# Kernel optimization log

Measured on AMD Instinct MI355X. Metric: run time of the kernel, lower is better.

The kernel has to match this reference:

```python
import jax, jax.numpy as jnp
import numpy as np

N = 100000       # nodes
E = 1600000      # edges (avg degree 16)
F_IN, H, C = 128, 128, 47


def setup_inputs() -> dict:
    key = jax.random.key(0)
    ks = jax.random.split(key, 12)
    def lin(k, fan_in, fan_out):
        return (jax.random.normal(k, (fan_in, fan_out), dtype=jnp.float32)
                / np.float32(np.sqrt(fan_in)))
    return {
        "x": jax.random.normal(ks[0], (N, F_IN), dtype=jnp.float32),
        "src": jax.random.randint(ks[1], (E,), 0, N, dtype=jnp.int32),
        "dst": jax.random.randint(ks[2], (E,), 0, N, dtype=jnp.int32),
        "w_self0": lin(ks[3], F_IN, H),
        "w_neigh0": lin(ks[4], F_IN, H),
        "b0": jnp.zeros((H,), jnp.float32),
        "w_self1": lin(ks[5], H, H),
        "w_neigh1": lin(ks[6], H, H),
        "b1": jnp.zeros((H,), jnp.float32),
        "w_self2": lin(ks[7], H, C),
        "w_neigh2": lin(ks[8], H, C),
        "b2": jnp.zeros((C,), jnp.float32),
    }


def _sage_layer(h, src, dst, w_self, w_neigh, b):
    # mean-aggregate neighbor features: gather h[src], scatter-add to dst
    agg = jax.ops.segment_sum(h[src], dst, num_segments=N)        # [N, d]
    deg = jax.ops.segment_sum(jnp.ones((src.shape[0], 1), h.dtype), dst,
                              num_segments=N)                     # [N, 1]
    mean = agg / jnp.maximum(deg, 1.0)
    # DGL SAGEConv('mean'): fc_self(h_dst) + fc_neigh(mean) + bias
    return h @ w_self + mean @ w_neigh + b


def reference(x, src, dst,
              w_self0, w_neigh0, b0,
              w_self1, w_neigh1, b1,
              w_self2, w_neigh2, b2):
    h = _sage_layer(x, src, dst, w_self0, w_neigh0, b0)
    h = jax.nn.relu(h)  # dropout is identity in eval mode
    h = _sage_layer(h, src, dst, w_self1, w_neigh1, b1)
    h = jax.nn.relu(h)
    h = _sage_layer(h, src, dst, w_self2, w_neigh2, b2)
    return h
```

## Files before the change

### kernel.cpp

```cpp
#include <hip/hip_runtime.h>

typedef unsigned int u32;
typedef unsigned short u16;
typedef __attribute__((ext_vector_type(8))) short short8;
typedef __attribute__((ext_vector_type(4))) float f32x4;

#define POOLCAP 65536
#define IDXMASK 0x1ffff

__device__ __forceinline__ u16 f2bf(float f) {
    u32 u = __float_as_uint(f);
    u32 r = (u + 0x7fffu + ((u >> 16) & 1u)) >> 16;
    return (u16)r;
}
__device__ __forceinline__ float bf2f(u32 lo16) { return __uint_as_float(lo16 << 16); }

__device__ __forceinline__ void acc_u4p(float2* a, uint4 v) {
    u32 w[4] = {v.x, v.y, v.z, v.w};
#pragma unroll
    for (int i = 0; i < 4; i++) {
        a[i].x += __uint_as_float(w[i] << 16);
        a[i].y += __uint_as_float(w[i] & 0xffff0000u);
    }
}


__global__ __launch_bounds__(256) void prep_w_all(const float* __restrict__ ws0, const float* __restrict__ wn0, u16* __restrict__ wt0,
                                                  const float* __restrict__ ws1, const float* __restrict__ wn1, u16* __restrict__ wt1,
                                                  const float* __restrict__ ws2, const float* __restrict__ wn2, u16* __restrict__ wt2) {
    int bid = blockIdx.x;
    const float *ws, *wn;
    u16* wt;
    int dout, HW, local;
    if (bid < 128)      { ws = ws0; wn = wn0; wt = wt0; dout = 128; HW = 128; local = bid; }
    else if (bid < 256) { ws = ws1; wn = wn1; wt = wt1; dout = 128; HW = 128; local = bid - 128; }
    else                { ws = ws2; wn = wn2; wt = wt2; dout = 47;  HW = 64;  local = bid - 256; }
    int idx = local * 256 + threadIdx.x;
    int n = idx >> 7, k = idx & 127;
    float v = 0.f;
    if (n < HW) { if (n < dout) v = ws[k * dout + n]; }
    else { int nn = n - HW; if (nn < dout) v = wn[k * dout + nn]; }
    wt[idx] = f2bf(v);
}


__global__ __launch_bounds__(256) void hist256(const int* __restrict__ dst,
                                               int* __restrict__ bcnt, int E) {
    __shared__ int bins[256];
    bins[threadIdx.x] = 0;
    __syncthreads();
    int gid = blockIdx.x * 256 + threadIdx.x;
    int stride = gridDim.x * 256;
    const int4* d4 = (const int4*)dst;
    int n4 = E >> 2;
    for (int k = gid; k < n4; k += stride) {
        int4 v = d4[k];
        atomicAdd(&bins[v.x >> 9], 1);
        atomicAdd(&bins[v.y >> 9], 1);
        atomicAdd(&bins[v.z >> 9], 1);
        atomicAdd(&bins[v.w >> 9], 1);
    }
    for (int k = (n4 << 2) + gid; k < E; k += stride)
        atomicAdd(&bins[dst[k] >> 9], 1);
    __syncthreads();
    int b = bins[threadIdx.x];
    if (b) atomicAdd(&bcnt[threadIdx.x], b);
}

__global__ __launch_bounds__(256) void scan256(const int* __restrict__ bcnt,
                                               int* __restrict__ boff,
                                               int* __restrict__ cursor) {
    __shared__ int sm[256];
    int t = threadIdx.x;
    int v = bcnt[t];
    sm[t] = v;
    __syncthreads();
    for (int off = 1; off < 256; off <<= 1) {
        int u = (t >= off) ? sm[t - off] : 0;
        __syncthreads();
        sm[t] += u;
        __syncthreads();
    }
    int excl = sm[t] - v;
    boff[t] = excl;
    cursor[t] = excl;
    if (t == 255) boff[256] = sm[255];
}

#define TILE 4096
__global__ __launch_bounds__(512) void bucket_scatter(const int* __restrict__ src,
                                                      const int* __restrict__ dst,
                                                      int* __restrict__ cursor,
                                                      uint2* __restrict__ pairs, int E) {
    __shared__ uint2 sp[TILE];
    __shared__ int s_cnt[256], s_off[256], s_gpos[256], s_cnt2[256];
    const int tid = threadIdx.x;
    const int base = blockIdx.x * TILE;
    const int tn = min(TILE, E - base);
    if (tid < 256) { s_cnt[tid] = 0; s_cnt2[tid] = 0; }
    __syncthreads();
    int d[8], s[8];
#pragma unroll
    for (int j = 0; j < 8; j++) {
        int k = tid + j * 512;
        if (k < tn) {
            d[j] = dst[base + k];
            s[j] = src[base + k];
            atomicAdd(&s_cnt[d[j] >> 9], 1);
        } else d[j] = -1;
    }
    __syncthreads();
    if (tid < 256) s_off[tid] = s_cnt[tid];
    __syncthreads();
    for (int off = 1; off < 256; off <<= 1) {
        int v = 0;
        if (tid < 256 && tid >= off) v = s_off[tid - off];
        __syncthreads();
        if (tid < 256) s_off[tid] += v;
        __syncthreads();
    }
    if (tid < 256 && s_cnt[tid] > 0) s_gpos[tid] = atomicAdd(&cursor[tid], s_cnt[tid]);
    __syncthreads();
#pragma unroll
    for (int j = 0; j < 8; j++) {
        if (d[j] >= 0) {
            int b = d[j] >> 9;
            int p = atomicAdd(&s_cnt2[b], 1);
            sp[s_off[b] - s_cnt[b] + p] = make_uint2((u32)d[j], (u32)s[j]);
        }
    }
    __syncthreads();
    for (int k = tid; k < tn; k += 512) {
        uint2 pr = sp[k];
        int b = (int)(pr.x >> 9);
        pairs[s_gpos[b] + (k - (s_off[b] - s_cnt[b]))] = pr;
    }
}

#define LDSCAP 12288
__global__ __launch_bounds__(512) void build_csr3(const uint2* __restrict__ pairs,
                                                  const int* __restrict__ boff,
                                                  float* __restrict__ invd,
                                                  int* __restrict__ colsF,
                                                  uint2* __restrict__ pool,
                                                  int* __restrict__ gcnt,
                                                  int Nn) {
    __shared__ int s_pack[LDSCAP];
    __shared__ int s_fix[512 * 32];
    __shared__ int s_cnt[512];
    const int tid = threadIdx.x;
    const int d0 = blockIdx.x * 512;
    const int nd = min(512, Nn - d0);
    const int base = boff[blockIdx.x];
    const int n = boff[blockIdx.x + 1] - base;
    const bool fit = (n <= LDSCAP);
    s_cnt[tid] = 0;
    {
        int4 sv4 = make_int4(Nn, Nn, Nn, Nn);
        int4* p4 = (int4*)s_fix;
        for (int k = tid; k < 512 * 32 / 4; k += 512) p4[k] = sv4;
    }
    __syncthreads();
    if (fit) {
        for (int k = tid; k < n; k += 512) {
            uint2 pr = pairs[base + k];
            int dl = (int)pr.x - d0;
            atomicAdd(&s_cnt[dl], 1);
            s_pack[k] = (dl << 17) | (int)pr.y;
        }
    } else {
        for (int k = tid; k < n; k += 512) {
            uint2 pr = pairs[base + k];
            atomicAdd(&s_cnt[(int)pr.x - d0], 1);
        }
    }
    __syncthreads();
    if (tid < nd) invd[d0 + tid] = 1.0f / (float)max(s_cnt[tid], 1);
    s_cnt[tid] = 0;
    __syncthreads();
    if (fit) {
        for (int k = tid; k < n; k += 512) {
            int pk = s_pack[k];
            int dl = pk >> 17, sc = pk & IDXMASK;
            int p = atomicAdd(&s_cnt[dl], 1);
            if (p < 32) s_fix[dl * 32 + p] = sc;
            else {
                int q = atomicAdd(gcnt, 1);
                if (q < POOLCAP) pool[q] = make_uint2((u32)(d0 + dl), (u32)sc);
            }
        }
    } else {
        for (int k = tid; k < n; k += 512) {
            uint2 pr = pairs[base + k];
            int dl = (int)pr.x - d0;
            int p = atomicAdd(&s_cnt[dl], 1);
            if (p < 32) s_fix[dl * 32 + p] = (int)pr.y;
            else {
                int q = atomicAdd(gcnt, 1);
                if (q < POOLCAP) pool[q] = make_uint2((u32)(d0 + dl), pr.y);
            }
        }
    }
    __syncthreads();
    int4* dst4 = (int4*)(colsF + (size_t)d0 * 32);
    const int4* s4p = (const int4*)s_fix;
    for (int k = tid; k < 512 * 32 / 4; k += 512) {
        int4 v = s4p[k];
        int dg = min(s_cnt[k >> 3], 0x7fff) << 17;
        v.x |= dg; v.y |= dg; v.z |= dg; v.w |= dg;
        dst4[k] = v;
    }
}

#define KDIM 128
#define KP 136

template <int NCOLS, bool AF32>
__global__ __launch_bounds__(256) void gemm_bf16(const void* __restrict__ Ap,
                                                 const u16* __restrict__ Bt,
                                                 u16* __restrict__ C, int M) {
    __shared__ u16 As[64 * KP];
    __shared__ u16 Bs[128 * KP];
    const int row0 = blockIdx.x * 64;
    const int col0 = blockIdx.y * 128;
    const int tid = threadIdx.x;

#pragma unroll
    for (int i = 0; i < 4; i++) {
        int idx = tid + i * 256;
        int r = idx >> 4, c = idx & 15;
        uint4 v = make_uint4(0, 0, 0, 0);
        if (row0 + r < M) {
            if (AF32) {
                const float* Af = (const float*)Ap;
                const float4* rowp = (const float4*)(Af + (size_t)(row0 + r) * KDIM);
                float4 f0 = rowp[2 * c];
                float4 f1 = rowp[2 * c + 1];
                v.x = (u32)f2bf(f0.x) | ((u32)f2bf(f0.y) << 16);
                v.y = (u32)f2bf(f0.z) | ((u32)f2bf(f0.w) << 16);
                v.z = (u32)f2bf(f1.x) | ((u32)f2bf(f1.y) << 16);
                v.w = (u32)f2bf(f1.z) | ((u32)f2bf(f1.w) << 16);
            } else {
                const u16* Ab = (const u16*)Ap;
                v = ((const uint4*)(Ab + (size_t)(row0 + r) * KDIM))[c];
            }
        }
        ((uint4*)(As + r * KP))[c] = v;
    }
#pragma unroll
    for (int i = 0; i < 8; i++) {
        int idx = tid + i * 256;
        int r = idx >> 4, c = idx & 15;
        uint4 v = ((const uint4*)(Bt + (size_t)(col0 + r) * KDIM))[c];
        ((uint4*)(Bs + r * KP))[c] = v;
    }
    __syncthreads();

    const int lane = tid & 63, wave = tid >> 6;
    const int quad = lane >> 4, l16 = lane & 15;
    const int wcol = wave * 32;

    f32x4 acc[4][2];
#pragma unroll
    for (int mt = 0; mt < 4; mt++)
#pragma unroll
        for (int nt = 0; nt < 2; nt++) acc[mt][nt] = (f32x4){0.f, 0.f, 0.f, 0.f};

#pragma unroll
    for (int kc = 0; kc < 4; kc++) {
        short8 a[4], b[2];
#pragma unroll
        for (int mt = 0; mt < 4; mt++)
            a[mt] = *(const short8*)(As + (size_t)(mt * 16 + l16) * KP + kc * 32 + quad * 8);
#pragma unroll
        for (int nt = 0; nt < 2; nt++)
            b[nt] = *(const short8*)(Bs + (size_t)(wcol + nt * 16 + l16) * KP + kc * 32 + quad * 8);
#pragma unroll
        for (int mt = 0; mt < 4; mt++)
#pragma unroll
            for (int nt = 0; nt < 2; nt++)
                acc[mt][nt] = __builtin_amdgcn_mfma_f32_16x16x32_bf16(a[mt], b[nt], acc[mt][nt], 0, 0, 0);
    }

    __syncthreads();
#pragma unroll
    for (int mt = 0; mt < 4; mt++)
#pragma unroll
        for (int i = 0; i < 4; i++) {
            int rl = mt * 16 + quad * 4 + i;
#pragma unroll
            for (int nt = 0; nt < 2; nt++)
                As[rl * KP + wcol + nt * 16 + l16] = f2bf(acc[mt][nt][i]);
        }
    __syncthreads();
#pragma unroll
    for (int it = 0; it < 4; it++) {
        int idx = tid + it * 256;
        int r = idx >> 4, c8 = idx & 15;
        if (row0 + r < M)
            *(uint4*)(C + (size_t)(row0 + r) * NCOLS + col0 + c8 * 8) =
                *(const uint4*)(As + r * KP + c8 * 8);
    }
}

template <bool RELU>
__global__ __launch_bounds__(256) void agg128f_k(const u16* __restrict__ out2,
                                                 const int* __restrict__ colsF,
                                                 const float* __restrict__ invd,
                                                 const float* __restrict__ bias,
                                                 u16* __restrict__ outp, int Mn) {
    int wave = threadIdx.x >> 6, lane = threadIdx.x & 63;
    int node = blockIdx.x * 4 + wave;
    if (node >= Mn) return;
    int sub = lane >> 4, l16 = lane & 15;
    const u16* tb = out2 + 128 + 8 * l16;
    const int* cp = colsF + node * 32 + sub;
    int s0 = cp[0],  s1 = cp[4],  s2 = cp[8],  s3 = cp[12];
    int s4 = cp[16], s5 = cp[20], s6 = cp[24], s7 = cp[28];
    const int deg = __builtin_amdgcn_readfirstlane(s0 >> 17);
    s0 &= IDXMASK; s1 &= IDXMASK; s2 &= IDXMASK; s3 &= IDXMASK;
    s4 &= IDXMASK; s5 &= IDXMASK; s6 &= IDXMASK; s7 &= IDXMASK;
    float id = invd[node];
    uint4 sv = *(const uint4*)(out2 + (size_t)node * 256 + 8 * l16);
    float4 b0 = *(const float4*)(bias + 8 * l16);
    float4 b1 = *(const float4*)(bias + 8 * l16 + 4);
    uint4 v0 = *(const uint4*)(tb + (size_t)s0 * 256);
    uint4 v1 = *(const uint4*)(tb + (size_t)s1 * 256);
    uint4 v2 = *(const uint4*)(tb + (size_t)s2 * 256);
    uint4 v3 = *(const uint4*)(tb + (size_t)s3 * 256);
    uint4 v4 = *(const uint4*)(tb + (size_t)s4 * 256);
    uint4 v5 = *(const uint4*)(tb + (size_t)s5 * 256);
    uint4 v6 = *(const uint4*)(tb + (size_t)s6 * 256);
    uint4 v7 = *(const uint4*)(tb + (size_t)s7 * 256);
    float2 a[4];
#pragma unroll
    for (int i = 0; i < 4; i++) a[i] = make_float2(0.f, 0.f);
    acc_u4p(a, v0);
    if (deg > 4)  acc_u4p(a, v1);
    if (deg > 8)  acc_u4p(a, v2);
    if (deg > 12) acc_u4p(a, v3);
    if (deg > 16) {
        acc_u4p(a, v4);
        if (deg > 20) acc_u4p(a, v5);
        if (deg > 24) acc_u4p(a, v6);
        if (deg > 28) acc_u4p(a, v7);
    }
    float af[8] = {a[0].x, a[0].y, a[1].x, a[1].y, a[2].x, a[2].y, a[3].x, a[3].y};
#pragma unroll
    for (int j = 0; j < 8; j++) {
        af[j] += __shfl_xor(af[j], 16); af[j] += __shfl_xor(af[j], 32);
    }
    if (sub == 0) {
        float o0 = bf2f(sv.x & 0xffffu) + af[0] * id + b0.x;
        float o1 = bf2f(sv.x >> 16)     + af[1] * id + b0.y;
        float o2 = bf2f(sv.y & 0xffffu) + af[2] * id + b0.z;
        float o3 = bf2f(sv.y >> 16)     + af[3] * id + b0.w;
        float o4 = bf2f(sv.z & 0xffffu) + af[4] * id + b1.x;
        float o5 = bf2f(sv.z >> 16)     + af[5] * id + b1.y;
        float o6 = bf2f(sv.w & 0xffffu) + af[6] * id + b1.z;
        float o7 = bf2f(sv.w >> 16)     + af[7] * id + b1.w;
        if (RELU) {
            o0 = fmaxf(o0, 0.f); o1 = fmaxf(o1, 0.f); o2 = fmaxf(o2, 0.f); o3 = fmaxf(o3, 0.f);
            o4 = fmaxf(o4, 0.f); o5 = fmaxf(o5, 0.f); o6 = fmaxf(o6, 0.f); o7 = fmaxf(o7, 0.f);
        }
        uint4 w;
        w.x = (u32)f2bf(o0) | ((u32)f2bf(o1) << 16);
        w.y = (u32)f2bf(o2) | ((u32)f2bf(o3) << 16);
        w.z = (u32)f2bf(o4) | ((u32)f2bf(o5) << 16);
        w.w = (u32)f2bf(o6) | ((u32)f2bf(o7) << 16);
        *(uint4*)(outp + (size_t)node * 128 + 8 * l16) = w;
    }
}

__global__ __launch_bounds__(256) void agg_out8f_k(const u16* __restrict__ out2,
                                                   const int* __restrict__ colsF,
                                                   const float* __restrict__ invd,
                                                   const float* __restrict__ bias,
                                                   float* __restrict__ outp, int Mn) {
    int wave = threadIdx.x >> 6, lane = threadIdx.x & 63;
    int node = blockIdx.x * 4 + wave;
    if (node >= Mn) return;
    int e8 = lane >> 3, l8 = lane & 7;
    const u16* tb = out2 + 64 + 8 * l8;
    const int* cp = colsF + node * 32 + e8;
    int s0 = cp[0], s1 = cp[8], s2 = cp[16], s3 = cp[24];
    const int deg = __builtin_amdgcn_readfirstlane(s0 >> 17);
    s0 &= IDXMASK; s1 &= IDXMASK; s2 &= IDXMASK; s3 &= IDXMASK;
    float id = invd[node];
    uint4 sv = *(const uint4*)(out2 + (size_t)node * 128 + 8 * l8);
    uint4 v0 = *(const uint4*)(tb + (size_t)s0 * 128);
    uint4 v1 = *(const uint4*)(tb + (size_t)s1 * 128);
    uint4 v2 = *(const uint4*)(tb + (size_t)s2 * 128);
    uint4 v3 = *(const uint4*)(tb + (size_t)s3 * 128);
    float2 a[4];
#pragma unroll
    for (int i = 0; i < 4; i++) a[i] = make_float2(0.f, 0.f);
    acc_u4p(a, v0);
    if (deg > 8)  acc_u4p(a, v1);
    if (deg > 16) acc_u4p(a, v2);
    if (deg > 24) acc_u4p(a, v3);
    float af[8] = {a[0].x, a[0].y, a[1].x, a[1].y, a[2].x, a[2].y, a[3].x, a[3].y};
#pragma unroll
    for (int j = 0; j < 8; j++) {
        af[j] += __shfl_xor(af[j], 8); af[j] += __shfl_xor(af[j], 16); af[j] += __shfl_xor(af[j], 32);
    }
    if (e8 == 0) {
        u32 sw[4] = {sv.x, sv.y, sv.z, sv.w};
        float* orow = outp + (size_t)node * 47;
#pragma unroll
        for (int j = 0; j < 8; j++) {
            int c = 8 * l8 + j;
            if (c < 47) {
                float s = bf2f((j & 1) ? (sw[j >> 1] >> 16) : (sw[j >> 1] & 0xffffu));
                orow[c] = s + af[j] * id + bias[c];
            }
        }
    }
}

template <int MODE>
__global__ __launch_bounds__(256) void oflow_k(const uint2* __restrict__ pool,
                                               const int* __restrict__ gcnt,
                                               const int* __restrict__ colsF,
                                               const u16* __restrict__ out2,
                                               const float* __restrict__ invd,
                                               const float* __restrict__ bias,
                                               void* __restrict__ outp, int Mn) {
    int cnt = min(*gcnt, POOLCAP);
    int wid = blockIdx.x * 4 + (threadIdx.x >> 6);
    int lane = threadIdx.x & 63;
    int nw = gridDim.x * 4;
    for (int i = wid; i < cnt; i += nw) {
        int node = (int)pool[i].x;
        float id = invd[node];
        if (MODE == 0) {
            int sub = lane >> 4, l16 = lane & 15;
            const u16* tb = out2 + 128 + 8 * l16;
            float2 a[4];
#pragma unroll
            for (int q = 0; q < 4; q++) a[q] = make_float2(0.f, 0.f);
#pragma unroll
            for (int k = 0; k < 8; k++) {
                int s = colsF[node * 32 + sub + 4 * k] & IDXMASK;
                acc_u4p(a, *(const uint4*)(tb + (size_t)s * 256));
            }
            for (int j = 0; j < cnt; j++) {
                uint2 pe = pool[j];
                if ((int)pe.x == node && sub == (j & 3))
                    acc_u4p(a, *(const uint4*)(tb + (size_t)pe.y * 256));
            }
            float af[8] = {a[0].x, a[0].y, a[1].x, a[1].y, a[2].x, a[2].y, a[3].x, a[3].y};
#pragma unroll
            for (int j = 0; j < 8; j++) {
                af[j] += __shfl_xor(af[j], 16); af[j] += __shfl_xor(af[j], 32);
            }
            if (sub == 0) {
                uint4 sv = *(const uint4*)(out2 + (size_t)node * 256 + 8 * l16);
                float4 b0 = *(const float4*)(bias + 8 * l16);
                float4 b1 = *(const float4*)(bias + 8 * l16 + 4);
                float o0 = bf2f(sv.x & 0xffffu) + af[0] * id + b0.x;
                float o1 = bf2f(sv.x >> 16)     + af[1] * id + b0.y;
                float o2 = bf2f(sv.y & 0xffffu) + af[2] * id + b0.z;
                float o3 = bf2f(sv.y >> 16)     + af[3] * id + b0.w;
                float o4 = bf2f(sv.z & 0xffffu) + af[4] * id + b1.x;
                float o5 = bf2f(sv.z >> 16)     + af[5] * id + b1.y;
                float o6 = bf2f(sv.w & 0xffffu) + af[6] * id + b1.z;
                float o7 = bf2f(sv.w >> 16)     + af[7] * id + b1.w;
                o0 = fmaxf(o0, 0.f); o1 = fmaxf(o1, 0.f); o2 = fmaxf(o2, 0.f); o3 = fmaxf(o3, 0.f);
                o4 = fmaxf(o4, 0.f); o5 = fmaxf(o5, 0.f); o6 = fmaxf(o6, 0.f); o7 = fmaxf(o7, 0.f);
                uint4 w;
                w.x = (u32)f2bf(o0) | ((u32)f2bf(o1) << 16);
                w.y = (u32)f2bf(o2) | ((u32)f2bf(o3) << 16);
                w.z = (u32)f2bf(o4) | ((u32)f2bf(o5) << 16);
                w.w = (u32)f2bf(o6) | ((u32)f2bf(o7) << 16);
                *(uint4*)((u16*)outp + (size_t)node * 128 + 8 * l16) = w;
            }
        } else {
            int e8 = lane >> 3, l8 = lane & 7;
            const u16* tb = out2 + 64 + 8 * l8;
            float2 a[4];
#pragma unroll
            for (int q = 0; q < 4; q++) a[q] = make_float2(0.f, 0.f);
#pragma unroll
            for (int k = 0; k < 4; k++) {
                int s = colsF[node * 32 + e8 + 8 * k] & IDXMASK;
                acc_u4p(a, *(const uint4*)(tb + (size_t)s * 128));
            }
            for (int j = 0; j < cnt; j++) {
                uint2 pe = pool[j];
                if ((int)pe.x == node && e8 == (j & 7))
                    acc_u4p(a, *(const uint4*)(tb + (size_t)pe.y * 128));
            }
            float af[8] = {a[0].x, a[0].y, a[1].x, a[1].y, a[2].x, a[2].y, a[3].x, a[3].y};
#pragma unroll
            for (int j = 0; j < 8; j++) {
                af[j] += __shfl_xor(af[j], 8); af[j] += __shfl_xor(af[j], 16); af[j] += __shfl_xor(af[j], 32);
            }
            if (e8 == 0) {
                uint4 sv = *(const uint4*)(out2 + (size_t)node * 128 + 8 * l8);
                u32 sw[4] = {sv.x, sv.y, sv.z, sv.w};
                float* orow = (float*)outp + (size_t)node * 47;
#pragma unroll
                for (int j = 0; j < 8; j++) {
                    int c = 8 * l8 + j;
                    if (c < 47) {
                        float s = bf2f((j & 1) ? (sw[j >> 1] >> 16) : (sw[j >> 1] & 0xffffu));
                        orow[c] = s + af[j] * id + bias[c];
                    }
                }
            }
        }
    }
}


extern "C" void kernel_launch(void* const* d_in, const int* in_sizes, int n_in,
                              void* d_out, int out_size, void* d_ws, size_t ws_size,
                              hipStream_t stream) {
    const float* x   = (const float*)d_in[0];
    const int*   src = (const int*)d_in[1];
    const int*   dst = (const int*)d_in[2];
    const float* ws0 = (const float*)d_in[3];
    const float* wn0 = (const float*)d_in[4];
    const float* b0  = (const float*)d_in[5];
    const float* ws1 = (const float*)d_in[6];
    const float* wn1 = (const float*)d_in[7];
    const float* b1  = (const float*)d_in[8];
    const float* ws2 = (const float*)d_in[9];
    const float* wn2 = (const float*)d_in[10];
    const float* b2  = (const float*)d_in[11];

    const int Nn = in_sizes[0] / 128;
    const int E  = in_sizes[1];
    const int nBuckets = (Nn + 511) / 512;
    const int NnPad = nBuckets * 512;

    char* p = (char*)d_ws;
    auto alloc = [&](size_t bytes) -> void* {
        void* r = (void*)p;
        p += (bytes + 255) & ~(size_t)255;
        return r;
    };
    u16*   bufA   = (u16*)alloc((size_t)Nn * 128 * 2);
    u16*   out2   = (u16*)alloc(((size_t)Nn * 256 + 256) * 2);
    u16*   wt0    = (u16*)alloc(256 * 128 * 2);
    u16*   wt1    = (u16*)alloc(256 * 128 * 2);
    u16*   wt2    = (u16*)alloc(128 * 128 * 2);
    float* invd   = (float*)alloc((size_t)Nn * 4);
    int*   colsF  = (int*)alloc((size_t)NnPad * 32 * 4);
    uint2* pool   = (uint2*)alloc((size_t)POOLCAP * 8);
    int*   gcnt   = (int*)alloc(256);
    int*   bcnt   = (int*)alloc(256 * 4);
    int*   boff   = (int*)alloc(257 * 4);
    int*   cursor = (int*)alloc(256 * 4);
    uint2* pairs  = (uint2*)out2;

    hipMemsetAsync(bcnt, 0, 256 * 4, stream);
    hipMemsetAsync(gcnt, 0, 4, stream);
    hipMemsetAsync(out2 + (size_t)Nn * 256, 0, 512, stream);

    prep_w_all<<<320, 256, 0, stream>>>(ws0, wn0, wt0, ws1, wn1, wt1, ws2, wn2, wt2);

    hist256<<<512, 256, 0, stream>>>(dst, bcnt, E);
    scan256<<<1, 256, 0, stream>>>(bcnt, boff, cursor);

    bucket_scatter<<<(E + TILE - 1) / TILE, 512, 0, stream>>>(src, dst, cursor, pairs, E);
    build_csr3<<<nBuckets, 512, 0, stream>>>(pairs, boff, invd, colsF, pool, gcnt, Nn);

    dim3 ggrid((Nn + 63) / 64, 2);
    dim3 ggrid1((Nn + 63) / 64, 1);
    const int aggGrid = (Nn + 3) / 4;
    gemm_bf16<256, true><<<ggrid, 256, 0, stream>>>(x, wt0, out2, Nn);
    agg128f_k<true><<<aggGrid, 256, 0, stream>>>(out2, colsF, invd, b0, bufA, Nn);
    oflow_k<0><<<8, 256, 0, stream>>>(pool, gcnt, colsF, out2, invd, b0, bufA, Nn);
    gemm_bf16<256, false><<<ggrid, 256, 0, stream>>>(bufA, wt1, out2, Nn);
    agg128f_k<true><<<aggGrid, 256, 0, stream>>>(out2, colsF, invd, b1, bufA, Nn);
    oflow_k<0><<<8, 256, 0, stream>>>(pool, gcnt, colsF, out2, invd, b1, bufA, Nn);
    gemm_bf16<128, false><<<ggrid1, 256, 0, stream>>>(bufA, wt2, out2, Nn);
    hipMemsetAsync(out2 + (size_t)Nn * 128, 0, 256, stream);
    agg_out8f_k<<<aggGrid, 256, 0, stream>>>(out2, colsF, invd, b2, (float*)d_out, Nn);
    oflow_k<1><<<8, 256, 0, stream>>>(pool, gcnt, colsF, out2, invd, b2, d_out, Nn);
}
```

Measured before the change: 413.1 us.

## Fuse overflow handling into aggregation kernels and simplify CSR build to one pass

Merges weight prep and the destination histogram into one launch, and folds the separate overflow kernels into the main aggregation kernels. Nodes with degree above 32 now scan the overflow pool inline. The CSR builder drops its two-pass LDS staging and writes slots in a single pass, padding unused entries at write-out. This removes several kernel launches and one pass over the edge pairs. In exchange, high-degree waves do a serial scan of the whole pool inside the main kernel, which can stall those waves.

```diff
diff --git a/kernel.cpp b/kernel.cpp
--- a/kernel.cpp
+++ b/kernel.cpp
@@ -25,32 +25,32 @@
 }
 
 
-__global__ __launch_bounds__(256) void prep_w_all(const float* __restrict__ ws0, const float* __restrict__ wn0, u16* __restrict__ wt0,
-                                                  const float* __restrict__ ws1, const float* __restrict__ wn1, u16* __restrict__ wt1,
-                                                  const float* __restrict__ ws2, const float* __restrict__ wn2, u16* __restrict__ wt2) {
+__global__ __launch_bounds__(256) void prep_hist(const float* __restrict__ ws0, const float* __restrict__ wn0, u16* __restrict__ wt0,
+                                                 const float* __restrict__ ws1, const float* __restrict__ wn1, u16* __restrict__ wt1,
+                                                 const float* __restrict__ ws2, const float* __restrict__ wn2, u16* __restrict__ wt2,
+                                                 const int* __restrict__ dst, int* __restrict__ bcnt, int E) {
+    __shared__ int bins[256];
     int bid = blockIdx.x;
-    const float *ws, *wn;
-    u16* wt;
-    int dout, HW, local;
-    if (bid < 128)      { ws = ws0; wn = wn0; wt = wt0; dout = 128; HW = 128; local = bid; }
-    else if (bid < 256) { ws = ws1; wn = wn1; wt = wt1; dout = 128; HW = 128; local = bid - 128; }
-    else                { ws = ws2; wn = wn2; wt = wt2; dout = 47;  HW = 64;  local = bid - 256; }
-    int idx = local * 256 + threadIdx.x;
-    int n = idx >> 7, k = idx & 127;
-    float v = 0.f;
-    if (n < HW) { if (n < dout) v = ws[k * dout + n]; }
-    else { int nn = n - HW; if (nn < dout) v = wn[k * dout + nn]; }
-    wt[idx] = f2bf(v);
-}
-
-
-__global__ __launch_bounds__(256) void hist256(const int* __restrict__ dst,
-                                               int* __restrict__ bcnt, int E) {
-    __shared__ int bins[256];
+    if (bid < 320) {
+        const float *ws, *wn;
+        u16* wt;
+        int dout, HW, local;
+        if (bid < 128)      { ws = ws0; wn = wn0; wt = wt0; dout = 128; HW = 128; local = bid; }
+        else if (bid < 256) { ws = ws1; wn = wn1; wt = wt1; dout = 128; HW = 128; local = bid - 128; }
+        else                { ws = ws2; wn = wn2; wt = wt2; dout = 47;  HW = 64;  local = bid - 256; }
+        int idx = local * 256 + threadIdx.x;
+        int n = idx >> 7, k = idx & 127;
+        float v = 0.f;
+        if (n < HW) { if (n < dout) v = ws[k * dout + n]; }
+        else { int nn = n - HW; if (nn < dout) v = wn[k * dout + nn]; }
+        wt[idx] = f2bf(v);
+        return;
+    }
     bins[threadIdx.x] = 0;
     __syncthreads();
-    int gid = blockIdx.x * 256 + threadIdx.x;
-    int stride = gridDim.x * 256;
+    int hb = bid - 320;
+    int gid = hb * 256 + threadIdx.x;
+    int stride = 512 * 256;
     const int4* d4 = (const int4*)dst;
     int n4 = E >> 2;
     for (int k = gid; k < n4; k += stride) {
@@ -137,7 +137,6 @@
     }
 }
 
-#define LDSCAP 12288
 __global__ __launch_bounds__(512) void build_csr3(const uint2* __restrict__ pairs,
                                                   const int* __restrict__ boff,
                                                   float* __restrict__ invd,
@@ -145,7 +144,6 @@
                                                   uint2* __restrict__ pool,
                                                   int* __restrict__ gcnt,
                                                   int Nn) {
-    __shared__ int s_pack[LDSCAP];
     __shared__ int s_fix[512 * 32];
     __shared__ int s_cnt[512];
     const int tid = threadIdx.x;
@@ -153,61 +151,31 @@
     const int nd = min(512, Nn - d0);
     const int base = boff[blockIdx.x];
     const int n = boff[blockIdx.x + 1] - base;
-    const bool fit = (n <= LDSCAP);
     s_cnt[tid] = 0;
-    {
-        int4 sv4 = make_int4(Nn, Nn, Nn, Nn);
-        int4* p4 = (int4*)s_fix;
-        for (int k = tid; k < 512 * 32 / 4; k += 512) p4[k] = sv4;
-    }
-    __syncthreads();
-    if (fit) {
-        for (int k = tid; k < n; k += 512) {
-            uint2 pr = pairs[base + k];
-            int dl = (int)pr.x - d0;
-            atomicAdd(&s_cnt[dl], 1);
-            s_pack[k] = (dl << 17) | (int)pr.y;
-        }
-    } else {
-        for (int k = tid; k < n; k += 512) {
-            uint2 pr = pairs[base + k];
-            atomicAdd(&s_cnt[(int)pr.x - d0], 1);
+    __syncthreads();
+    for (int k = tid; k < n; k += 512) {
+        uint2 pr = pairs[base + k];
+        int dl = (int)pr.x - d0;
+        int p = atomicAdd(&s_cnt[dl], 1);
+        if (p < 32) s_fix[dl * 32 + p] = (int)pr.y;
+        else {
+            int q = atomicAdd(gcnt, 1);
+            if (q < POOLCAP) pool[q] = make_uint2(pr.x, pr.y);
         }
     }
     __syncthreads();
     if (tid < nd) invd[d0 + tid] = 1.0f / (float)max(s_cnt[tid], 1);
-    s_cnt[tid] = 0;
-    __syncthreads();
-    if (fit) {
-        for (int k = tid; k < n; k += 512) {
-            int pk = s_pack[k];
-            int dl = pk >> 17, sc = pk & IDXMASK;
-            int p = atomicAdd(&s_cnt[dl], 1);
-            if (p < 32) s_fix[dl * 32 + p] = sc;
-            else {
-                int q = atomicAdd(gcnt, 1);
-                if (q < POOLCAP) pool[q] = make_uint2((u32)(d0 + dl), (u32)sc);
-            }
-        }
-    } else {
-        for (int k = tid; k < n; k += 512) {
-            uint2 pr = pairs[base + k];
-            int dl = (int)pr.x - d0;
-            int p = atomicAdd(&s_cnt[dl], 1);
-            if (p < 32) s_fix[dl * 32 + p] = (int)pr.y;
-            else {
-                int q = atomicAdd(gcnt, 1);
-                if (q < POOLCAP) pool[q] = make_uint2((u32)(d0 + dl), pr.y);
-            }
-        }
-    }
-    __syncthreads();
     int4* dst4 = (int4*)(colsF + (size_t)d0 * 32);
-    const int4* s4p = (const int4*)s_fix;
     for (int k = tid; k < 512 * 32 / 4; k += 512) {
-        int4 v = s4p[k];
-        int dg = min(s_cnt[k >> 3], 0x7fff) << 17;
-        v.x |= dg; v.y |= dg; v.z |= dg; v.w |= dg;
+        int node = k >> 3;
+        int cnt = s_cnt[node];
+        int dg = min(cnt, 0x7fff) << 17;
+        int sb = (k & 7) * 4;
+        int4 v;
+        v.x = ((sb + 0 < cnt) ? s_fix[k * 4 + 0] : Nn) | dg;
+        v.y = ((sb + 1 < cnt) ? s_fix[k * 4 + 1] : Nn) | dg;
+        v.z = ((sb + 2 < cnt) ? s_fix[k * 4 + 2] : Nn) | dg;
+        v.w = ((sb + 3 < cnt) ? s_fix[k * 4 + 3] : Nn) | dg;
         dst4[k] = v;
     }
 }
@@ -308,6 +276,8 @@
                                                  const int* __restrict__ colsF,
                                                  const float* __restrict__ invd,
                                                  const float* __restrict__ bias,
+                                                 const uint2* __restrict__ pool,
+                                                 const int* __restrict__ gcnt,
                                                  u16* __restrict__ outp, int Mn) {
     int wave = threadIdx.x >> 6, lane = threadIdx.x & 63;
     int node = blockIdx.x * 4 + wave;
@@ -345,6 +315,14 @@
         if (deg > 24) acc_u4p(a, v6);
         if (deg > 28) acc_u4p(a, v7);
     }
+    if (deg > 32) {
+        int cnt = min(*gcnt, POOLCAP);
+        for (int j = 0; j < cnt; j++) {
+            uint2 pe = pool[j];
+            if ((int)pe.x == node && sub == (j & 3))
+                acc_u4p(a, *(const uint4*)(tb + (size_t)pe.y * 256));
+        }
+    }
     float af[8] = {a[0].x, a[0].y, a[1].x, a[1].y, a[2].x, a[2].y, a[3].x, a[3].y};
 #pragma unroll
     for (int j = 0; j < 8; j++) {
@@ -376,6 +354,8 @@
                                                    const int* __restrict__ colsF,
                                                    const float* __restrict__ invd,
                                                    const float* __restrict__ bias,
+                                                   const uint2* __restrict__ pool,
+                                                   const int* __restrict__ gcnt,
                                                    float* __restrict__ outp, int Mn) {
     int wave = threadIdx.x >> 6, lane = threadIdx.x & 63;
     int node = blockIdx.x * 4 + wave;
@@ -399,6 +379,14 @@
     if (deg > 8)  acc_u4p(a, v1);
     if (deg > 16) acc_u4p(a, v2);
     if (deg > 24) acc_u4p(a, v3);
+    if (deg > 32) {
+        int cnt = min(*gcnt, POOLCAP);
+        for (int j = 0; j < cnt; j++) {
+            uint2 pe = pool[j];
+            if ((int)pe.x == node && e8 == (j & 7))
+                acc_u4p(a, *(const uint4*)(tb + (size_t)pe.y * 128));
+        }
+    }
     float af[8] = {a[0].x, a[0].y, a[1].x, a[1].y, a[2].x, a[2].y, a[3].x, a[3].y};
 #pragma unroll
     for (int j = 0; j < 8; j++) {
@@ -413,101 +401,6 @@
             if (c < 47) {
                 float s = bf2f((j & 1) ? (sw[j >> 1] >> 16) : (sw[j >> 1] & 0xffffu));
                 orow[c] = s + af[j] * id + bias[c];
-            }
-        }
-    }
-}
-
-template <int MODE>
-__global__ __launch_bounds__(256) void oflow_k(const uint2* __restrict__ pool,
-                                               const int* __restrict__ gcnt,
-                                               const int* __restrict__ colsF,
-                                               const u16* __restrict__ out2,
-                                               const float* __restrict__ invd,
-                                               const float* __restrict__ bias,
-                                               void* __restrict__ outp, int Mn) {
-    int cnt = min(*gcnt, POOLCAP);
-    int wid = blockIdx.x * 4 + (threadIdx.x >> 6);
-    int lane = threadIdx.x & 63;
-    int nw = gridDim.x * 4;
-    for (int i = wid; i < cnt; i += nw) {
-        int node = (int)pool[i].x;
-        float id = invd[node];
-        if (MODE == 0) {
-            int sub = lane >> 4, l16 = lane & 15;
-            const u16* tb = out2 + 128 + 8 * l16;
-            float2 a[4];
-#pragma unroll
-            for (int q = 0; q < 4; q++) a[q] = make_float2(0.f, 0.f);
-#pragma unroll
-            for (int k = 0; k < 8; k++) {
-                int s = colsF[node * 32 + sub + 4 * k] & IDXMASK;
-                acc_u4p(a, *(const uint4*)(tb + (size_t)s * 256));
-            }
-            for (int j = 0; j < cnt; j++) {
-                uint2 pe = pool[j];
-                if ((int)pe.x == node && sub == (j & 3))
-                    acc_u4p(a, *(const uint4*)(tb + (size_t)pe.y * 256));
-            }
-            float af[8] = {a[0].x, a[0].y, a[1].x, a[1].y, a[2].x, a[2].y, a[3].x, a[3].y};
-#pragma unroll
-            for (int j = 0; j < 8; j++) {
-                af[j] += __shfl_xor(af[j], 16); af[j] += __shfl_xor(af[j], 32);
-            }
-            if (sub == 0) {
-                uint4 sv = *(const uint4*)(out2 + (size_t)node * 256 + 8 * l16);
-                float4 b0 = *(const float4*)(bias + 8 * l16);
-                float4 b1 = *(const float4*)(bias + 8 * l16 + 4);
-                float o0 = bf2f(sv.x & 0xffffu) + af[0] * id + b0.x;
-                float o1 = bf2f(sv.x >> 16)     + af[1] * id + b0.y;
-                float o2 = bf2f(sv.y & 0xffffu) + af[2] * id + b0.z;
-                float o3 = bf2f(sv.y >> 16)     + af[3] * id + b0.w;
-                float o4 = bf2f(sv.z & 0xffffu) + af[4] * id + b1.x;
-                float o5 = bf2f(sv.z >> 16)     + af[5] * id + b1.y;
-                float o6 = bf2f(sv.w & 0xffffu) + af[6] * id + b1.z;
-                float o7 = bf2f(sv.w >> 16)     + af[7] * id + b1.w;
-                o0 = fmaxf(o0, 0.f); o1 = fmaxf(o1, 0.f); o2 = fmaxf(o2, 0.f); o3 = fmaxf(o3, 0.f);
-                o4 = fmaxf(o4, 0.f); o5 = fmaxf(o5, 0.f); o6 = fmaxf(o6, 0.f); o7 = fmaxf(o7, 0.f);
-                uint4 w;
-                w.x = (u32)f2bf(o0) | ((u32)f2bf(o1) << 16);
-                w.y = (u32)f2bf(o2) | ((u32)f2bf(o3) << 16);
-                w.z = (u32)f2bf(o4) | ((u32)f2bf(o5) << 16);
-                w.w = (u32)f2bf(o6) | ((u32)f2bf(o7) << 16);
-                *(uint4*)((u16*)outp + (size_t)node * 128 + 8 * l16) = w;
-            }
-        } else {
-            int e8 = lane >> 3, l8 = lane & 7;
-            const u16* tb = out2 + 64 + 8 * l8;
-            float2 a[4];
-#pragma unroll
-            for (int q = 0; q < 4; q++) a[q] = make_float2(0.f, 0.f);
-#pragma unroll
-            for (int k = 0; k < 4; k++) {
-                int s = colsF[node * 32 + e8 + 8 * k] & IDXMASK;
-                acc_u4p(a, *(const uint4*)(tb + (size_t)s * 128));
-            }
-            for (int j = 0; j < cnt; j++) {
-                uint2 pe = pool[j];
-                if ((int)pe.x == node && e8 == (j & 7))
-                    acc_u4p(a, *(const uint4*)(tb + (size_t)pe.y * 128));
-            }
-            float af[8] = {a[0].x, a[0].y, a[1].x, a[1].y, a[2].x, a[2].y, a[3].x, a[3].y};
-#pragma unroll
-            for (int j = 0; j < 8; j++) {
-                af[j] += __shfl_xor(af[j], 8); af[j] += __shfl_xor(af[j], 16); af[j] += __shfl_xor(af[j], 32);
-            }
-            if (e8 == 0) {
-                uint4 sv = *(const uint4*)(out2 + (size_t)node * 128 + 8 * l8);
-                u32 sw[4] = {sv.x, sv.y, sv.z, sv.w};
-                float* orow = (float*)outp + (size_t)node * 47;
-#pragma unroll
-                for (int j = 0; j < 8; j++) {
-                    int c = 8 * l8 + j;
-                    if (c < 47) {
-                        float s = bf2f((j & 1) ? (sw[j >> 1] >> 16) : (sw[j >> 1] & 0xffffu));
-                        orow[c] = s + af[j] * id + bias[c];
-                    }
-                }
             }
         }
     }
@@ -559,9 +452,8 @@
     hipMemsetAsync(gcnt, 0, 4, stream);
     hipMemsetAsync(out2 + (size_t)Nn * 256, 0, 512, stream);
 
-    prep_w_all<<<320, 256, 0, stream>>>(ws0, wn0, wt0, ws1, wn1, wt1, ws2, wn2, wt2);
-
-    hist256<<<512, 256, 0, stream>>>(dst, bcnt, E);
+    prep_hist<<<832, 256, 0, stream>>>(ws0, wn0, wt0, ws1, wn1, wt1, ws2, wn2, wt2,
+                                       dst, bcnt, E);
     scan256<<<1, 256, 0, stream>>>(bcnt, boff, cursor);
 
     bucket_scatter<<<(E + TILE - 1) / TILE, 512, 0, stream>>>(src, dst, cursor, pairs, E);
@@ -571,13 +463,10 @@
     dim3 ggrid1((Nn + 63) / 64, 1);
     const int aggGrid = (Nn + 3) / 4;
     gemm_bf16<256, true><<<ggrid, 256, 0, stream>>>(x, wt0, out2, Nn);
-    agg128f_k<true><<<aggGrid, 256, 0, stream>>>(out2, colsF, invd, b0, bufA, Nn);
-    oflow_k<0><<<8, 256, 0, stream>>>(pool, gcnt, colsF, out2, invd, b0, bufA, Nn);
+    agg128f_k<true><<<aggGrid, 256, 0, stream>>>(out2, colsF, invd, b0, pool, gcnt, bufA, Nn);
     gemm_bf16<256, false><<<ggrid, 256, 0, stream>>>(bufA, wt1, out2, Nn);
-    agg128f_k<true><<<aggGrid, 256, 0, stream>>>(out2, colsF, invd, b1, bufA, Nn);
-    oflow_k<0><<<8, 256, 0, stream>>>(pool, gcnt, colsF, out2, invd, b1, bufA, Nn);
+    agg128f_k<true><<<aggGrid, 256, 0, stream>>>(out2, colsF, invd, b1, pool, gcnt, bufA, Nn);
     gemm_bf16<128, false><<<ggrid1, 256, 0, stream>>>(bufA, wt2, out2, Nn);
     hipMemsetAsync(out2 + (size_t)Nn * 128, 0, 256, stream);
-    agg_out8f_k<<<aggGrid, 256, 0, stream>>>(out2, colsF, invd, b2, (float*)d_out, Nn);
-    oflow_k<1><<<8, 256, 0, stream>>>(pool, gcnt, colsF, out2, invd, b2, d_out, Nn);
-}
+    agg_out8f_k<<<aggGrid, 256, 0, stream>>>(out2, colsF, invd, b2, pool, gcnt, (float*)d_out, Nn);
+}
```

New measurement: 388.8 us. 5.9% less time.
